# Kernel tuning notes

Measured on AMD Instinct MI355X. Metric: run time of the kernel, lower is better.

## Reference

```python
import jax, jax.numpy as jnp
import numpy as np

B, S, E, H = 8, 1024, 1024, 16  # batch, seq, embed, heads; head_dim = E//H = 64

def setup_inputs() -> dict:
    key = jax.random.key(0)
    k1, k2, k3 = jax.random.split(key, 3)
    x = jax.random.normal(k1, (B, S, E), dtype=jnp.float32)
    W_attn = jax.random.normal(k2, (E, 3 * E), dtype=jnp.float32) * (1.0 / np.sqrt(E))
    W_proj = jax.random.normal(k3, (E, E), dtype=jnp.float32) * (1.0 / np.sqrt(E))
    return {"x": x, "W_attn": W_attn, "W_proj": W_proj}

def reference(x, W_attn, W_proj):
    b, s, e = x.shape
    d = e // H
    qkv = x @ W_attn                      # [b, s, 3e]
    q, k, v = jnp.split(qkv, 3, axis=-1)
    q = q.reshape(b, s, H, d)
    k = k.reshape(b, s, H, d)
    v = v.reshape(b, s, H, d)
    scale = 1.0 / np.sqrt(d).astype(np.float32)
    scores = jnp.einsum('bqhd,bkhd->bhqk', q, k) * scale  # [b, H, s, s]
    causal = jnp.tril(jnp.ones((s, s), dtype=bool))
    scores = jnp.where(causal[None, None, :, :], scores, -jnp.inf)
    attn = jax.nn.softmax(scores, axis=-1)
    y = jnp.einsum('bhqk,bkhd->bqhd', attn, v).reshape(b, s, e)
    return y @ W_proj
```

## Files before the change

kernel.cpp:

```cpp
#include <hip/hip_runtime.h>
#include <hip/hip_bf16.h>

typedef unsigned short u16;
typedef __attribute__((ext_vector_type(8))) short short8;
typedef __attribute__((ext_vector_type(4))) float f32x4;
typedef __attribute__((ext_vector_type(16))) float f32x16;
typedef __attribute__((ext_vector_type(4))) unsigned short u16x4;

#define DEVINL __device__ __forceinline__

DEVINL u16 f2bf(float f) {
    union { float f; unsigned u; } x; x.f = f;
    unsigned u = x.u;
    u += 0x7fffu + ((u >> 16) & 1u);
    return (u16)(u >> 16);
}

DEVINL void gload_lds16(const void* g, void* l) {
    __builtin_amdgcn_global_load_lds(
        (const __attribute__((address_space(1))) unsigned*)g,
        (__attribute__((address_space(3))) unsigned*)l, 16, 0, 0);
}

DEVINL int swz(int row) { return (((row & 7) ^ ((row >> 3) & 7)) << 4); }

DEVINL void swap32(unsigned& a, unsigned& b) {
#if __has_builtin(__builtin_amdgcn_permlane32_swap)
    typedef __attribute__((ext_vector_type(2))) unsigned uv2;
    uv2 r = __builtin_amdgcn_permlane32_swap(a, b, false, false);
    a = r.x; b = r.y;
#else
    int h = ((int)(threadIdx.x & 63)) >> 5;
    unsigned pa = (unsigned)__shfl_xor((int)a, 32);
    unsigned pb = (unsigned)__shfl_xor((int)b, 32);
    unsigned na = h ? pb : a;
    unsigned nb = h ? b : pa;
    a = na; b = nb;
#endif
}

__global__ void k_conv_x(const float* __restrict__ in, u16* __restrict__ out, int n4) {
    int i = blockIdx.x * blockDim.x + threadIdx.x;
    int stride = gridDim.x * blockDim.x;
    for (; i < n4; i += stride) {
        float4 v = ((const float4*)in)[i];
        u16x4 o;
        o.x = f2bf(v.x); o.y = f2bf(v.y); o.z = f2bf(v.z); o.w = f2bf(v.w);
        ((u16x4*)out)[i] = o;
    }
}

__global__ void k_transpose_bf(const float* __restrict__ in, u16* __restrict__ out, int R, int C) {
    __shared__ float t[32][33];
    int c0 = blockIdx.x * 32, r0 = blockIdx.y * 32;
    int tx = threadIdx.x, ty = threadIdx.y;
    #pragma unroll
    for (int j = 0; j < 32; j += 8)
        t[ty + j][tx] = in[(size_t)(r0 + ty + j) * C + c0 + tx];
    __syncthreads();
    #pragma unroll
    for (int j = 0; j < 32; j += 8)
        out[(size_t)(c0 + ty + j) * R + r0 + tx] = f2bf(t[tx][ty + j]);
}

template<bool OUT_BF16>
__global__ __launch_bounds__(256, 2)
void k_gemm_bt(const u16* __restrict__ A, const u16* __restrict__ BT,
               void* __restrict__ C, int N, int K) {
    __shared__ u16 Asm[128 * 32];
    __shared__ u16 Bsm[128 * 32];
    const int tid  = threadIdx.x;
    const int lane = tid & 63;
    const int wave = tid >> 6;

    const int gx   = gridDim.x;
    const int nwg  = gx * gridDim.y;
    const int orig = blockIdx.y * gx + blockIdx.x;
    const int wg   = (orig & 7) * (nwg >> 3) + (orig >> 3);
    const int bx   = wg % gx;
    const int by   = wg / gx;

    const long row0 = (long)by * 128;
    const long col0 = (long)bx * 128;
    const int  wr = (wave >> 1) * 64;
    const int  wc = (wave & 1) * 64;

    f32x4 acc[4][4] = {};

    const int ar0 = lane >> 2;
    const int ak  = (lane & 3) * 8;

    for (int kb = 0; kb < K; kb += 32) {
        #pragma unroll
        for (int i = 0; i < 2; i++) {
            int ch = wave * 2 + i;
            int r  = ch * 16 + ar0;
            gload_lds16(A  + (row0 + r) * (size_t)K + kb + ak, &Asm[ch * 512]);
            gload_lds16(BT + (col0 + r) * (size_t)K + kb + ak, &Bsm[ch * 512]);
        }
        __syncthreads();
        short8 af[4], bfr[4];
        #pragma unroll
        for (int m = 0; m < 4; m++)
            af[m] = *(const short8*)&Asm[(wr + m * 16 + (lane & 15)) * 32 + (lane >> 4) * 8];
        #pragma unroll
        for (int n = 0; n < 4; n++)
            bfr[n] = *(const short8*)&Bsm[(wc + n * 16 + (lane & 15)) * 32 + (lane >> 4) * 8];
        #pragma unroll
        for (int m = 0; m < 4; m++)
            #pragma unroll
            for (int n = 0; n < 4; n++)
                acc[m][n] = __builtin_amdgcn_mfma_f32_16x16x32_bf16(af[m], bfr[n], acc[m][n], 0, 0, 0);
        __syncthreads();
    }

    const int rl = (lane >> 4) * 4;
    const int cl = lane & 15;
    #pragma unroll
    for (int m = 0; m < 4; m++)
        #pragma unroll
        for (int n = 0; n < 4; n++)
            #pragma unroll
            for (int r = 0; r < 4; r++) {
                long row = row0 + wr + m * 16 + rl + r;
                long col = col0 + wc + n * 16 + cl;
                if constexpr (OUT_BF16)
                    ((u16*)C)[row * (size_t)N + col] = f2bf(acc[m][n][r]);
                else
                    ((float*)C)[row * (size_t)N + col] = acc[m][n][r];
            }
}

#define SCALE_L2E 0.18033688011112042f

__global__ __launch_bounds__(256, 2)
void k_attn(const u16* __restrict__ qkv, u16* __restrict__ y) {
    constexpr int S = 1024, E = 1024, TE = 3072;
    __shared__ u16 Kt[64 * 64];
    __shared__ u16 Vt[64 * 64];

    const int tid  = threadIdx.x;
    const int lane = tid & 63;
    const int l31  = lane & 31;
    const int hA   = lane >> 5;
    const int wave = tid >> 6;

    const int qi = 7 - (int)(blockIdx.x >> 7);
    const int bh = blockIdx.x & 127;
    const int b  = bh >> 4;
    const int h  = bh & 15;
    const int q0 = qi * 128;
    const size_t rowbase = (size_t)b * S;
    const int qg = q0 + wave * 32 + l31;

    short8 qf[4];
    {
        const u16* qp = qkv + (rowbase + qg) * TE + h * 64 + hA * 8;
        #pragma unroll
        for (int kd = 0; kd < 4; kd++) qf[kd] = *(const short8*)(qp + kd * 16);
    }

    f32x16 o0 = {}, o1 = {};
    float ms = -1e30f, lsum = 0.f;

    const int kr0 = (wave << 3) + (lane >> 3);
    const int kcb = (lane & 7) * 16;
    const int vkv = (tid >> 3) * 2;
    const int vdc = (tid & 7) * 8;

    const int ntiles = 2 * qi + 2;
    for (int t = 0; t < ntiles; ++t) {
        const int kv0 = t * 64;
        __syncthreads();
        #pragma unroll
        for (int it = 0; it < 2; it++) {
            int r = kr0 + it * 32;
            const char* src = (const char*)qkv
                + (((rowbase + kv0 + r) * TE + E + h * 64) << 1) + (kcb ^ swz(r));
            gload_lds16(src, (char*)Kt + wave * 1024 + it * 4096);
        }
        {
            const u16* vsrc = qkv + (rowbase + kv0 + vkv) * TE + 2 * E + h * 64 + vdc;
            short8 v0 = *(const short8*)vsrc;
            short8 v1 = *(const short8*)(vsrc + TE);
            #pragma unroll
            for (int j = 0; j < 8; j++) {
                int d = vdc + j;
                unsigned val = (unsigned)(u16)v0[j] | ((unsigned)(u16)v1[j] << 16);
                *(unsigned*)((char*)Vt + d * 128 + ((vkv * 2) ^ swz(d))) = val;
            }
        }
        __syncthreads();

        const bool active = (kv0 <= q0 + wave * 32 + 31);
        if (!active) continue;

        f32x16 s0 = {}, s1 = {};
        #pragma unroll
        for (int kd = 0; kd < 4; kd++) {
            int r0 = l31, r1 = 32 + l31;
            short8 ka0 = *(const short8*)((const char*)Kt + r0 * 128 + ((kd * 32 + hA * 16) ^ swz(r0)));
            short8 ka1 = *(const short8*)((const char*)Kt + r1 * 128 + ((kd * 32 + hA * 16) ^ swz(r1)));
            s0 = __builtin_amdgcn_mfma_f32_32x32x16_bf16(ka0, qf[kd], s0, 0, 0, 0);
            s1 = __builtin_amdgcn_mfma_f32_32x32x16_bf16(ka1, qf[kd], s1, 0, 0, 0);
        }

        if (kv0 + 63 > q0 + wave * 32) {
            #pragma unroll
            for (int r = 0; r < 16; r++) {
                int kvr = kv0 + ((r & 3) + 8 * (r >> 2) + 4 * hA);
                if (kvr > qg)      s0[r] = -1e30f;
                if (kvr + 32 > qg) s1[r] = -1e30f;
            }
        }

        float pm = s0[0];
        #pragma unroll
        for (int r = 1; r < 16; r++) pm = fmaxf(pm, s0[r]);
        #pragma unroll
        for (int r = 0; r < 16; r++) pm = fmaxf(pm, s1[r]);
        pm = fmaxf(pm, __shfl_xor(pm, 32));
        float pms = pm * SCALE_L2E;
        if (__any(pms - ms > 8.0f)) {
            float msn = fmaxf(ms, pms);
            float alpha = exp2f(ms - msn);
            ms = msn;
            lsum *= alpha;
            #pragma unroll
            for (int r = 0; r < 16; r++) { o0[r] *= alpha; o1[r] *= alpha; }
        }

        float part = 0.f;
        #pragma unroll
        for (int r = 0; r < 16; r++) {
            float p0 = exp2f(s0[r] * SCALE_L2E - ms);
            float p1 = exp2f(s1[r] * SCALE_L2E - ms);
            s0[r] = p0; s1[r] = p1;
            part += p0 + p1;
        }
        lsum += part + __shfl_xor(part, 32);

        unsigned w0[8], w1[8];
        #pragma unroll
        for (int j = 0; j < 8; j++) {
            asm("v_cvt_pk_bf16_f32 %0, %1, %2" : "=v"(w0[j]) : "v"(s0[2 * j]), "v"(s0[2 * j + 1]));
            asm("v_cvt_pk_bf16_f32 %0, %1, %2" : "=v"(w1[j]) : "v"(s1[2 * j]), "v"(s1[2 * j + 1]));
        }

        #define PV_TILE(W, ST)                                                              \
        {                                                                                   \
            _Pragma("unroll")                                                               \
            for (int kkl = 0; kkl < 2; kkl++) {                                             \
                unsigned a  = W[4 * kkl],     bsw = W[4 * kkl + 2];                         \
                unsigned a2 = W[4 * kkl + 1], b2  = W[4 * kkl + 3];                         \
                swap32(a, bsw); swap32(a2, b2);                                             \
                union { int4 i; short8 s; } u;                                              \
                u.i = make_int4((int)a, (int)a2, (int)bsw, (int)b2);                        \
                {                                                                           \
                    int row = l31;                                                          \
                    short8 va = *(const short8*)((const char*)Vt + row * 128                \
                                  + (((ST) * 64 + kkl * 32 + hA * 16) ^ swz(row)));         \
                    o0 = __builtin_amdgcn_mfma_f32_32x32x16_bf16(va, u.s, o0, 0, 0, 0);     \
                }                                                                           \
                {                                                                           \
                    int row = 32 + l31;                                                     \
                    short8 va = *(const short8*)((const char*)Vt + row * 128                \
                                  + (((ST) * 64 + kkl * 32 + hA * 16) ^ swz(row)));         \
                    o1 = __builtin_amdgcn_mfma_f32_32x32x16_bf16(va, u.s, o1, 0, 0, 0);     \
                }                                                                           \
            }                                                                               \
        }
        PV_TILE(w0, 0)
        PV_TILE(w1, 1)
        #undef PV_TILE
    }

    __syncthreads();
    float rinv = 1.0f / lsum;
    u16* Ot = (wave < 2 ? Kt : Vt) + (wave & 1) * 2048;
    const int X = (l31 & 7) << 4;
    #pragma unroll
    for (int rq = 0; rq < 4; rq++) {
        u16x4 pk0, pk1;
        #pragma unroll
        for (int j = 0; j < 4; j++) {
            pk0[j] = f2bf(o0[4 * rq + j] * rinv);
            pk1[j] = f2bf(o1[4 * rq + j] * rinv);
        }
        *(u16x4*)((char*)Ot + l31 * 128 + ((16 * rq + 8 * hA) ^ X))      = pk0;
        *(u16x4*)((char*)Ot + l31 * 128 + ((64 + 16 * rq + 8 * hA) ^ X)) = pk1;
    }
    __syncthreads();
    #pragma unroll
    for (int p = 0; p < 4; p++) {
        int row = p * 8 + (lane >> 3);
        int cc  = lane & 7;
        short8 vv = *(const short8*)((const char*)Ot + row * 128
                      + ((cc * 16) ^ ((row & 7) << 4)));
        *(short8*)(y + (rowbase + q0 + wave * 32 + row) * E + h * 64 + cc * 8) = vv;
    }
}

extern "C" void kernel_launch(void* const* d_in, const int* in_sizes, int n_in,
                              void* d_out, int out_size, void* d_ws, size_t ws_size,
                              hipStream_t stream) {
    const float* x     = (const float*)d_in[0];
    const float* Wattn = (const float*)d_in[1];
    const float* Wproj = (const float*)d_in[2];
    float* out = (float*)d_out;

    char* ws = (char*)d_ws;
    u16* buf0 = (u16*)ws;
    u16* wT   = (u16*)(ws + 16777216);
    u16* qkv  = (u16*)(ws + 16777216 + 6291456);

    k_conv_x<<<2048, 256, 0, stream>>>(x, buf0, 8388608 / 4);
    k_transpose_bf<<<dim3(3072 / 32, 1024 / 32), dim3(32, 8), 0, stream>>>(Wattn, wT, 1024, 3072);
    k_gemm_bt<true><<<dim3(3072 / 128, 8192 / 128), 256, 0, stream>>>(buf0, wT, qkv, 3072, 1024);
    k_transpose_bf<<<dim3(1024 / 32, 1024 / 32), dim3(32, 8), 0, stream>>>(Wproj, wT, 1024, 1024);
    k_attn<<<dim3(1024), 256, 0, stream>>>(qkv, buf0);
    k_gemm_bt<false><<<dim3(1024 / 128, 8192 / 128), 256, 0, stream>>>(buf0, wT, out, 1024, 1024);
}
```

Baseline: 149.5 us.

## Replace GEMM with triple-buffered, swizzled, larger-tile pipelined MFMA kernel

Replaces the single-buffered 128x128 GEMM with a templated kernel that uses 512 threads, larger tiles (256x256 for the QKV projection, 128x256 for the output projection), and a three-stage LDS ring. Global-to-LDS loads for step t+2 are issued while MFMAs run on step t, and partial vmcnt waits stand in for full barriers. An XOR swizzle on the LDS layout is meant to avoid bank conflicts, and s_setprio boosts the MFMA section. The cost is more LDS and registers per block, fewer blocks in the grid, and hand-written waitcnt counts that must match the number of loads per stage.

```diff
diff --git a/kernel.cpp b/kernel.cpp
--- a/kernel.cpp
+++ b/kernel.cpp
@@ -63,67 +63,110 @@
         out[(size_t)(c0 + ty + j) * R + r0 + tx] = f2bf(t[tx][ty + j]);
 }
 
-template<bool OUT_BF16>
-__global__ __launch_bounds__(256, 2)
-void k_gemm_bt(const u16* __restrict__ A, const u16* __restrict__ BT,
-               void* __restrict__ C, int N, int K) {
-    __shared__ u16 Asm[128 * 32];
-    __shared__ u16 Bsm[128 * 32];
+template<int BM, int BN, bool OUT_BF16>
+__global__ __launch_bounds__(512, 2)
+void k_gemm_p(const u16* __restrict__ A, const u16* __restrict__ BT,
+              void* __restrict__ C, int N, int K) {
+    constexpr int BK = 32;
+    constexpr int AI = BM / 128;
+    constexpr int BI = BN / 128;
+    constexpr int LOADS = AI + BI;
+    constexpr int MF = BM / 2 / 16;
+    constexpr int NF = BN / 4 / 16;
+    constexpr int ABYTES = BM * BK * 2;
+    constexpr int BBYTES = BN * BK * 2;
+    constexpr int TBYTES = ABYTES + BBYTES;
+    __shared__ char lds[3 * TBYTES];
+
     const int tid  = threadIdx.x;
     const int lane = tid & 63;
+    const int lo   = lane & 15;
+    const int hi   = lane >> 4;
     const int wave = tid >> 6;
+    const int wm   = wave >> 2;
+    const int wn   = wave & 3;
 
     const int gx   = gridDim.x;
     const int nwg  = gx * gridDim.y;
     const int orig = blockIdx.y * gx + blockIdx.x;
     const int wg   = (orig & 7) * (nwg >> 3) + (orig >> 3);
-    const int bx   = wg % gx;
-    const int by   = wg / gx;
-
-    const long row0 = (long)by * 128;
-    const long col0 = (long)bx * 128;
-    const int  wr = (wave >> 1) * 64;
-    const int  wc = (wave & 1) * 64;
-
-    f32x4 acc[4][4] = {};
-
-    const int ar0 = lane >> 2;
-    const int ak  = (lane & 3) * 8;
-
-    for (int kb = 0; kb < K; kb += 32) {
-        #pragma unroll
-        for (int i = 0; i < 2; i++) {
-            int ch = wave * 2 + i;
-            int r  = ch * 16 + ar0;
-            gload_lds16(A  + (row0 + r) * (size_t)K + kb + ak, &Asm[ch * 512]);
-            gload_lds16(BT + (col0 + r) * (size_t)K + kb + ak, &Bsm[ch * 512]);
-        }
-        __syncthreads();
-        short8 af[4], bfr[4];
-        #pragma unroll
-        for (int m = 0; m < 4; m++)
-            af[m] = *(const short8*)&Asm[(wr + m * 16 + (lane & 15)) * 32 + (lane >> 4) * 8];
-        #pragma unroll
-        for (int n = 0; n < 4; n++)
-            bfr[n] = *(const short8*)&Bsm[(wc + n * 16 + (lane & 15)) * 32 + (lane >> 4) * 8];
-        #pragma unroll
-        for (int m = 0; m < 4; m++)
-            #pragma unroll
-            for (int n = 0; n < 4; n++)
+    const long row0 = (long)(wg / gx) * BM;
+    const long col0 = (long)(wg % gx) * BN;
+
+    f32x4 acc[MF][NF] = {};
+
+    const int r0s = tid >> 2;
+    const int sl  = tid & 3;
+
+    const int NT = K >> 5;
+
+    auto stage = [&](int t) {
+        char* base = lds + (t % 3) * TBYTES;
+        const int kb = t * BK;
+        #pragma unroll
+        for (int i = 0; i < AI; i++) {
+            int r  = i * 128 + r0s;
+            int kc = sl ^ (r & 3);
+            gload_lds16(A + (row0 + r) * (size_t)K + kb + kc * 8,
+                        base + i * 8192 + tid * 16);
+        }
+        #pragma unroll
+        for (int i = 0; i < BI; i++) {
+            int r  = i * 128 + r0s;
+            int kc = sl ^ (r & 3);
+            gload_lds16(BT + (col0 + r) * (size_t)K + kb + kc * 8,
+                        base + ABYTES + i * 8192 + tid * 16);
+        }
+    };
+
+    stage(0);
+    stage(1);
+
+    for (int t = 0; t < NT; t++) {
+        if (t + 1 < NT) {
+            if constexpr (LOADS == 4) asm volatile("s_waitcnt vmcnt(4)" ::: "memory");
+            else                      asm volatile("s_waitcnt vmcnt(3)" ::: "memory");
+        } else {
+            asm volatile("s_waitcnt vmcnt(0)" ::: "memory");
+        }
+        __builtin_amdgcn_s_barrier();
+        __builtin_amdgcn_sched_barrier(0);
+
+        if (t + 2 < NT) stage(t + 2);
+
+        const char* ab = lds + (t % 3) * TBYTES;
+        const char* bb = ab + ABYTES;
+
+        short8 af[MF], bfr[NF];
+        #pragma unroll
+        for (int m = 0; m < MF; m++) {
+            int r = wm * (BM / 2) + m * 16 + lo;
+            af[m] = *(const short8*)(ab + r * 64 + ((hi * 16) ^ ((r & 3) << 4)));
+        }
+        #pragma unroll
+        for (int n = 0; n < NF; n++) {
+            int r = wn * (BN / 4) + n * 16 + lo;
+            bfr[n] = *(const short8*)(bb + r * 64 + ((hi * 16) ^ ((r & 3) << 4)));
+        }
+
+        __builtin_amdgcn_s_setprio(1);
+        #pragma unroll
+        for (int m = 0; m < MF; m++)
+            #pragma unroll
+            for (int n = 0; n < NF; n++)
                 acc[m][n] = __builtin_amdgcn_mfma_f32_16x16x32_bf16(af[m], bfr[n], acc[m][n], 0, 0, 0);
-        __syncthreads();
-    }
-
-    const int rl = (lane >> 4) * 4;
-    const int cl = lane & 15;
-    #pragma unroll
-    for (int m = 0; m < 4; m++)
-        #pragma unroll
-        for (int n = 0; n < 4; n++)
+        __builtin_amdgcn_s_setprio(0);
+    }
+
+    const int rl = hi * 4;
+    #pragma unroll
+    for (int m = 0; m < MF; m++)
+        #pragma unroll
+        for (int n = 0; n < NF; n++)
             #pragma unroll
             for (int r = 0; r < 4; r++) {
-                long row = row0 + wr + m * 16 + rl + r;
-                long col = col0 + wc + n * 16 + cl;
+                long row = row0 + wm * (BM / 2) + m * 16 + rl + r;
+                long col = col0 + wn * (BN / 4) + n * 16 + lo;
                 if constexpr (OUT_BF16)
                     ((u16*)C)[row * (size_t)N + col] = f2bf(acc[m][n][r]);
                 else
@@ -316,8 +359,8 @@
 
     k_conv_x<<<2048, 256, 0, stream>>>(x, buf0, 8388608 / 4);
     k_transpose_bf<<<dim3(3072 / 32, 1024 / 32), dim3(32, 8), 0, stream>>>(Wattn, wT, 1024, 3072);
-    k_gemm_bt<true><<<dim3(3072 / 128, 8192 / 128), 256, 0, stream>>>(buf0, wT, qkv, 3072, 1024);
+    k_gemm_p<256, 256, true><<<dim3(3072 / 256, 8192 / 256), 512, 0, stream>>>(buf0, wT, qkv, 3072, 1024);
     k_transpose_bf<<<dim3(1024 / 32, 1024 / 32), dim3(32, 8), 0, stream>>>(Wproj, wT, 1024, 1024);
     k_attn<<<dim3(1024), 256, 0, stream>>>(qkv, buf0);
-    k_gemm_bt<false><<<dim3(1024 / 128, 8192 / 128), 256, 0, stream>>>(buf0, wT, out, 1024, 1024);
-}
+    k_gemm_p<128, 256, false><<<dim3(1024 / 256, 8192 / 128), 512, 0, stream>>>(buf0, wT, out, 1024, 1024);
+}
```

Measured after the change: 151.4 us. About the same (+1.3%).

## Double-buffer GEMM LDS tiles with K=64 steps and XOR-swizzled layout

Applied to the files above, without the earlier changes.

Rewrites the bf16 GEMM used for the QKV and output projections. LDS is now double-buffered so the global-to-LDS load of the next K tile overlaps the MFMA work on the current one. The K step grows from 32 to 64, which halves the number of barriers, and an XOR swizzle on the LDS layout is meant to avoid bank conflicts on the fragment reads. LDS per block grows to 64KB, which may limit how many blocks fit per CU.

```diff
diff --git a/kernel.cpp b/kernel.cpp
--- a/kernel.cpp
+++ b/kernel.cpp
@@ -65,65 +65,85 @@
 
 template<bool OUT_BF16>
 __global__ __launch_bounds__(256, 2)
-void k_gemm_bt(const u16* __restrict__ A, const u16* __restrict__ BT,
-               void* __restrict__ C, int N, int K) {
-    __shared__ u16 Asm[128 * 32];
-    __shared__ u16 Bsm[128 * 32];
+void k_gemm2(const u16* __restrict__ A, const u16* __restrict__ BT,
+             void* __restrict__ C, int N, int K) {
+    __shared__ char lds[2 * 32768];
+
     const int tid  = threadIdx.x;
     const int lane = tid & 63;
+    const int lo   = lane & 15;
+    const int hi   = lane >> 4;
     const int wave = tid >> 6;
+    const int wm   = wave >> 1;
+    const int wn   = wave & 1;
 
     const int gx   = gridDim.x;
     const int nwg  = gx * gridDim.y;
     const int orig = blockIdx.y * gx + blockIdx.x;
     const int wg   = (orig & 7) * (nwg >> 3) + (orig >> 3);
-    const int bx   = wg % gx;
-    const int by   = wg / gx;
-
-    const long row0 = (long)by * 128;
-    const long col0 = (long)bx * 128;
-    const int  wr = (wave >> 1) * 64;
-    const int  wc = (wave & 1) * 64;
+    const long row0 = (long)(wg / gx) * 128;
+    const long col0 = (long)(wg % gx) * 128;
+
+    const int NT = K >> 6;
+
+    const int srow = tid >> 3;
+    const int gsb  = ((tid & 7) ^ (srow & 7)) << 4;
+
+    auto stage = [&](int t) {
+        char* base = lds + (t & 1) * 32768;
+        #pragma unroll
+        for (int c = 0; c < 4; c++)
+            gload_lds16((const char*)(A + (row0 + c * 32 + srow) * (size_t)K + t * 64) + gsb,
+                        base + c * 4096 + tid * 16);
+        #pragma unroll
+        for (int c = 0; c < 4; c++)
+            gload_lds16((const char*)(BT + (col0 + c * 32 + srow) * (size_t)K + t * 64) + gsb,
+                        base + 16384 + c * 4096 + tid * 16);
+    };
 
     f32x4 acc[4][4] = {};
 
-    const int ar0 = lane >> 2;
-    const int ak  = (lane & 3) * 8;
-
-    for (int kb = 0; kb < K; kb += 32) {
-        #pragma unroll
-        for (int i = 0; i < 2; i++) {
-            int ch = wave * 2 + i;
-            int r  = ch * 16 + ar0;
-            gload_lds16(A  + (row0 + r) * (size_t)K + kb + ak, &Asm[ch * 512]);
-            gload_lds16(BT + (col0 + r) * (size_t)K + kb + ak, &Bsm[ch * 512]);
-        }
-        __syncthreads();
-        short8 af[4], bfr[4];
-        #pragma unroll
-        for (int m = 0; m < 4; m++)
-            af[m] = *(const short8*)&Asm[(wr + m * 16 + (lane & 15)) * 32 + (lane >> 4) * 8];
+    stage(0);
+    asm volatile("s_waitcnt vmcnt(0)" ::: "memory");
+    __builtin_amdgcn_s_barrier();
+
+    for (int t = 0; t < NT; t++) {
+        if (t + 1 < NT) stage(t + 1);
+        const char* ab = lds + (t & 1) * 32768;
+        const char* bb = ab + 16384;
+        #pragma unroll
+        for (int kk = 0; kk < 2; kk++) {
+            short8 af[4], bf[4];
+            #pragma unroll
+            for (int m = 0; m < 4; m++) {
+                int r = wm * 64 + m * 16 + lo;
+                af[m] = *(const short8*)(ab + r * 128 + ((kk * 64 + hi * 16) ^ ((r & 7) << 4)));
+            }
+            #pragma unroll
+            for (int n = 0; n < 4; n++) {
+                int r = wn * 64 + n * 16 + lo;
+                bf[n] = *(const short8*)(bb + r * 128 + ((kk * 64 + hi * 16) ^ ((r & 7) << 4)));
+            }
+            #pragma unroll
+            for (int m = 0; m < 4; m++)
+                #pragma unroll
+                for (int n = 0; n < 4; n++)
+                    acc[m][n] = __builtin_amdgcn_mfma_f32_16x16x32_bf16(af[m], bf[n], acc[m][n], 0, 0, 0);
+        }
+        if (t + 1 < NT) {
+            asm volatile("s_waitcnt vmcnt(0)" ::: "memory");
+            __builtin_amdgcn_s_barrier();
+        }
+    }
+
+    #pragma unroll
+    for (int m = 0; m < 4; m++)
         #pragma unroll
         for (int n = 0; n < 4; n++)
-            bfr[n] = *(const short8*)&Bsm[(wc + n * 16 + (lane & 15)) * 32 + (lane >> 4) * 8];
-        #pragma unroll
-        for (int m = 0; m < 4; m++)
-            #pragma unroll
-            for (int n = 0; n < 4; n++)
-                acc[m][n] = __builtin_amdgcn_mfma_f32_16x16x32_bf16(af[m], bfr[n], acc[m][n], 0, 0, 0);
-        __syncthreads();
-    }
-
-    const int rl = (lane >> 4) * 4;
-    const int cl = lane & 15;
-    #pragma unroll
-    for (int m = 0; m < 4; m++)
-        #pragma unroll
-        for (int n = 0; n < 4; n++)
             #pragma unroll
             for (int r = 0; r < 4; r++) {
-                long row = row0 + wr + m * 16 + rl + r;
-                long col = col0 + wc + n * 16 + cl;
+                long row = row0 + wm * 64 + m * 16 + hi * 4 + r;
+                long col = col0 + wn * 64 + n * 16 + lo;
                 if constexpr (OUT_BF16)
                     ((u16*)C)[row * (size_t)N + col] = f2bf(acc[m][n][r]);
                 else
@@ -316,8 +336,8 @@
 
     k_conv_x<<<2048, 256, 0, stream>>>(x, buf0, 8388608 / 4);
     k_transpose_bf<<<dim3(3072 / 32, 1024 / 32), dim3(32, 8), 0, stream>>>(Wattn, wT, 1024, 3072);
-    k_gemm_bt<true><<<dim3(3072 / 128, 8192 / 128), 256, 0, stream>>>(buf0, wT, qkv, 3072, 1024);
+    k_gemm2<true><<<dim3(3072 / 128, 8192 / 128), 256, 0, stream>>>(buf0, wT, qkv, 3072, 1024);
     k_transpose_bf<<<dim3(1024 / 32, 1024 / 32), dim3(32, 8), 0, stream>>>(Wproj, wT, 1024, 1024);
     k_attn<<<dim3(1024), 256, 0, stream>>>(qkv, buf0);
-    k_gemm_bt<false><<<dim3(1024 / 128, 8192 / 128), 256, 0, stream>>>(buf0, wT, out, 1024, 1024);
-}
+    k_gemm2<false><<<dim3(1024 / 128, 8192 / 128), 256, 0, stream>>>(buf0, wT, out, 1024, 1024);
+}
```

Result: faster. 133.7 us (-10.6%).
